# Performance work log

Hardware: AMD Instinct MI355X
Metric: run time of the kernel (lower is better)

## Reference

```python
import jax, jax.numpy as jnp
import numpy as np

N_NODES = 100000


def gcn_conv(x, edge_index, edge_weight, W, b):
    """GCNConv with self-loops and symmetric normalization: D^-1/2 (A+I) D^-1/2 (xW) + b."""
    n = x.shape[0]
    h = x @ W  # [N, out]
    src, dst = edge_index[0], edge_index[1]
    loop = jnp.arange(n, dtype=edge_index.dtype)
    src_f = jnp.concatenate([src, loop])
    dst_f = jnp.concatenate([dst, loop])
    w_f = jnp.concatenate([edge_weight, jnp.ones((n,), dtype=edge_weight.dtype)])
    deg = jax.ops.segment_sum(w_f, dst_f, num_segments=n)  # in-degree incl. self-loop
    dinv = jnp.where(deg > 0, jax.lax.rsqrt(deg), 0.0)
    norm = dinv[src_f] * w_f * dinv[dst_f]  # [E+N]
    msg = norm[:, None] * h[src_f]  # gather + scale
    out = jax.ops.segment_sum(msg, dst_f, num_segments=n)  # scatter-add
    return out + b


def setup_inputs() -> dict:
    key = jax.random.key(0)
    k1, k2, k3, k4 = jax.random.split(key, 4)
    x = jax.random.normal(k1, (N_NODES, 512), dtype=jnp.float32)
    edge_index = jax.random.randint(k2, (2, 3200000), 0, N_NODES, dtype=jnp.int64)
    edge_weight = jnp.ones((3200000,), dtype=jnp.float32)
    W1 = jax.random.normal(k3, (512, 16), dtype=jnp.float32) * 0.05
    b1 = jnp.zeros((16,), dtype=jnp.float32)
    W2 = jax.random.normal(k4, (16, 7), dtype=jnp.float32) * 0.05
    b2 = jnp.zeros((7,), dtype=jnp.float32)
    return {"x": x, "edge_index": edge_index, "edge_weight": edge_weight,
            "W1": W1, "b1": b1, "W2": W2, "b2": b2}


def reference(x, edge_index, edge_weight, W1, b1, W2, b2):
    h = jax.nn.relu(gcn_conv(x, edge_index, edge_weight, W1, b1))
    # F.dropout(training=False) is identity at inference
    h = gcn_conv(h, edge_index, edge_weight, W2, b2)
    return jax.nn.log_softmax(h, axis=1)
```

## Files before the change

kernel.cpp:

```cpp
#include <hip/hip_runtime.h>
#include <hip/hip_fp16.h>
#include <math.h>


#define F0 512
#define F1 16
#define F2 7
#define NPB 128
#define NBMAX 1024
#define BINCAP 4800
#define CH 4096
#define CMAX 80


__global__ __launch_bounds__(1024) void k_init2(
        const int* __restrict__ ei32, int twoE, int* __restrict__ flag,
        int* __restrict__ gcnt) {
    int t = threadIdx.x;
    if (t < 64) {
        int idx = 1 + 2 * t;
        int v = (idx < twoE) ? ei32[idx] : 0;
        unsigned long long b = __ballot(v != 0);
        if (t == 0) *flag = (b == 0ULL) ? 1 : 0;
    }
    if (t < NBMAX) gcnt[t] = 0;
}

__global__ __launch_bounds__(512) void kA_bin(
        const int* __restrict__ ei32, const long long* __restrict__ ei64,
        const int* __restrict__ flag, const float* __restrict__ w,
        int* __restrict__ gcnt, int2* __restrict__ binrec, int E, int nbin) {
    __shared__ int2 sorted[CH];
    __shared__ unsigned short binof[CH];
    __shared__ int hist[NBMAX];
    __shared__ int scanb[NBMAX];
    __shared__ int basel[NBMAX];
    __shared__ int curb[NBMAX];
    int t = threadIdx.x;
    int base = blockIdx.x * CH;
    int cnt_c = E - base; if (cnt_c > CH) cnt_c = CH;
    for (int i = t; i < NBMAX; i += 512) { hist[i] = 0; curb[i] = 0; }
    __syncthreads();
    bool f64 = (*flag) != 0;
#pragma unroll
    for (int k = 0; k < CH / 512; ++k) {
        int li = t + k * 512;
        if (li < cnt_c) {
            int e = base + li;
            int dst = f64 ? (int)ei64[(size_t)E + e] : ei32[(size_t)E + e];
            atomicAdd(&hist[dst >> 7], 1);
        }
    }
    __syncthreads();
    scanb[t] = hist[t]; scanb[t + 512] = hist[t + 512];
    __syncthreads();
    for (int off = 1; off < NBMAX; off <<= 1) {
        int a0 = (t >= off) ? scanb[t - off] : 0;
        int a1 = scanb[t + 512 - off];
        __syncthreads();
        scanb[t] += a0; scanb[t + 512] += a1;
        __syncthreads();
    }
    {
        int e0 = scanb[t] - hist[t];
        int e1 = scanb[t + 512] - hist[t + 512];
        __syncthreads();
        scanb[t] = e0; scanb[t + 512] = e1;
        if (t < nbin)       basel[t]       = hist[t]       ? atomicAdd(&gcnt[t],       hist[t])       : 0;
        if (t + 512 < nbin) basel[t + 512] = hist[t + 512] ? atomicAdd(&gcnt[t + 512], hist[t + 512]) : 0;
    }
    __syncthreads();
#pragma unroll
    for (int k = 0; k < CH / 512; ++k) {
        int li = t + k * 512;
        if (li < cnt_c) {
            int e = base + li;
            int src, dst;
            if (f64) { src = (int)ei64[e]; dst = (int)ei64[(size_t)E + e]; }
            else     { src = ei32[e];      dst = ei32[(size_t)E + e]; }
            int b = dst >> 7;
            int r = atomicAdd(&curb[b], 1);
            int slot = scanb[b] + r;
            sorted[slot] = make_int2((src << 7) | (dst & 127),
                                     __float_as_int(w[e]));
            binof[slot] = (unsigned short)b;
        }
    }
    __syncthreads();
    for (int idx = t; idx < cnt_c; idx += 512) {
        int b = binof[idx];
        int pos = basel[b] + (idx - scanb[b]);
        if (pos < BINCAP)
            binrec[(size_t)b * BINCAP + pos] = sorted[idx];
    }
}

__global__ __launch_bounds__(1024) void kB_scanbins(
        const int* __restrict__ gcnt, int* __restrict__ gbase, int nbin) {
    __shared__ int s[NBMAX];
    int t = threadIdx.x;
    int v = 0;
    if (t < nbin) { v = gcnt[t]; if (v > BINCAP) v = BINCAP; }
    s[t] = v;
    __syncthreads();
    for (int off = 1; off < NBMAX; off <<= 1) {
        int a = (t >= off) ? s[t - off] : 0;
        __syncthreads();
        s[t] += a;
        __syncthreads();
    }
    if (t < nbin) gbase[t] = s[t] - v;
}

__global__ __launch_bounds__(512) void kB_build(
        const int2* __restrict__ binrec, const int* __restrict__ gcnt,
        const int* __restrict__ gbase, int2* __restrict__ ep,
        int* __restrict__ rp, int* __restrict__ cntn,
        float* __restrict__ dinv, int n) {
    __shared__ int2 rec[BINCAP];
    __shared__ int2 srt[BINCAP];
    __shared__ int hist[NPB];
    __shared__ float wsum[NPB];
    __shared__ int offl[NPB];
    __shared__ int curl[NPB];
    int bin = blockIdx.x;
    int t = threadIdx.x;
    int cb = gcnt[bin]; if (cb > BINCAP) cb = BINCAP;
    int gb = gbase[bin];
    if (t < NPB) { hist[t] = 0; wsum[t] = 0.f; curl[t] = 0; }
    __syncthreads();
    for (int i = t; i < cb; i += 512) {
        int2 r = binrec[(size_t)bin * BINCAP + i];
        rec[i] = r;
        int d = r.x & 127;
        atomicAdd(&hist[d], 1);
        atomicAdd(&wsum[d], __int_as_float(r.y));
    }
    __syncthreads();
    if (t < NPB) offl[t] = hist[t];
    __syncthreads();
    for (int off = 1; off < NPB; off <<= 1) {
        int a = 0;
        if (t < NPB && t >= off) a = offl[t - off];
        __syncthreads();
        if (t < NPB) offl[t] += a;
        __syncthreads();
    }
    if (t < NPB) {
        int excl = offl[t] - hist[t];
        int node = bin * NPB + t;
        if (node < n) {
            cntn[node] = hist[t];
            rp[node] = gb + excl;
            float d = 1.f + wsum[t];
            dinv[node] = (d > 0.f) ? rsqrtf(d) : 0.f;
        }
        offl[t] = excl;
    }
    __syncthreads();
    for (int i = t; i < cb; i += 512) {
        int2 r = rec[i];
        int d = r.x & 127;
        int slot = offl[d] + atomicAdd(&curl[d], 1);
        srt[slot] = make_int2((int)(((unsigned)r.x) >> 7), r.y);
    }
    __syncthreads();
    for (int i = t; i < cb; i += 512)
        ep[(size_t)gb + i] = srt[i];
}

__global__ __launch_bounds__(256) void k_gemm1(
        const float* __restrict__ x, const float* __restrict__ W1,
        const float* __restrict__ dinv, __half* __restrict__ h1, int n) {
    int row = blockIdx.x * 256 + threadIdx.x;
    if (row >= n) return;
    const float4* xr = (const float4*)(x + (size_t)row * F0);
    const float4* wb = (const float4*)W1;
    float acc[F1];
#pragma unroll
    for (int j = 0; j < F1; ++j) acc[j] = 0.f;
#pragma unroll 2
    for (int k4 = 0; k4 < F0 / 4; ++k4) {
        float4 xv = xr[k4];
        const float4* wr = wb + k4 * 16;
#pragma unroll
        for (int j4 = 0; j4 < 4; ++j4) {
            float4 w0 = wr[j4];
            float4 w1 = wr[4 + j4];
            float4 w2 = wr[8 + j4];
            float4 w3 = wr[12 + j4];
            acc[4*j4+0] = fmaf(xv.w, w3.x, fmaf(xv.z, w2.x, fmaf(xv.y, w1.x, fmaf(xv.x, w0.x, acc[4*j4+0]))));
            acc[4*j4+1] = fmaf(xv.w, w3.y, fmaf(xv.z, w2.y, fmaf(xv.y, w1.y, fmaf(xv.x, w0.y, acc[4*j4+1]))));
            acc[4*j4+2] = fmaf(xv.w, w3.z, fmaf(xv.z, w2.z, fmaf(xv.y, w1.z, fmaf(xv.x, w0.z, acc[4*j4+2]))));
            acc[4*j4+3] = fmaf(xv.w, w3.w, fmaf(xv.z, w2.w, fmaf(xv.y, w1.w, fmaf(xv.x, w0.w, acc[4*j4+3]))));
        }
    }
    float di = dinv[row];
    __half2 hp[8];
#pragma unroll
    for (int q = 0; q < 8; ++q)
        hp[q] = __floats2half2_rn(di * acc[2*q], di * acc[2*q+1]);
    int4 o0, o1;
    o0.x = *(int*)&hp[0]; o0.y = *(int*)&hp[1]; o0.z = *(int*)&hp[2]; o0.w = *(int*)&hp[3];
    o1.x = *(int*)&hp[4]; o1.y = *(int*)&hp[5]; o1.z = *(int*)&hp[6]; o1.w = *(int*)&hp[7];
    int4* o = (int4*)(h1 + (size_t)row * F1);
    o[0] = o0;
    o[1] = o1;
}

__global__ __launch_bounds__(256) void kg1(
        const int* __restrict__ rp, const int* __restrict__ cntn,
        const int2* __restrict__ ep, const __half* __restrict__ h1,
        const float* __restrict__ dinv, const float* __restrict__ b1,
        const float* __restrict__ W2, __half* __restrict__ h2, int n) {
    __shared__ float sW[F1 * 9];
    int t = threadIdx.x;
    if (t < F1 * 8) {
        int j = t >> 3, c = t & 7;
        sW[j * 9 + c] = (c < F2) ? W2[j * F2 + c] : 0.f;
    }
    __syncthreads();
    int node = blockIdx.x * 16 + (t >> 4);
    int j = t & 15;
    if (node >= n) return;
    int start = rp[node], c = cntn[node];
    const int2* b = ep + start;
    float a0 = 0.f, a1 = 0.f, a2 = 0.f, a3 = 0.f;
    int k = 0;
    for (; k + 3 < c; k += 4) {
        int2 p0 = b[k], p1 = b[k+1], p2 = b[k+2], p3 = b[k+3];
        a0 += __int_as_float(p0.y) * __half2float(h1[(size_t)p0.x * F1 + j]);
        a1 += __int_as_float(p1.y) * __half2float(h1[(size_t)p1.x * F1 + j]);
        a2 += __int_as_float(p2.y) * __half2float(h1[(size_t)p2.x * F1 + j]);
        a3 += __int_as_float(p3.y) * __half2float(h1[(size_t)p3.x * F1 + j]);
    }
    for (; k < c; ++k) {
        int2 p = b[k];
        a0 += __int_as_float(p.y) * __half2float(h1[(size_t)p.x * F1 + j]);
    }
    float di = dinv[node];
    float self = __half2float(h1[(size_t)node * F1 + j]);
    float g = di * ((a0 + a1) + (a2 + a3) + self) + b1[j];
    g = fmaxf(g, 0.f);
    float hv[8];
#pragma unroll
    for (int cc = 0; cc < 8; ++cc) hv[cc] = g * sW[j * 9 + cc];
#pragma unroll
    for (int off = 1; off < 16; off <<= 1) {
#pragma unroll
        for (int cc = 0; cc < 8; ++cc) hv[cc] += __shfl_xor(hv[cc], off, 16);
    }
    float o = hv[0];
#pragma unroll
    for (int cc = 1; cc < 8; ++cc) if (j == cc) o = hv[cc];
    if (j < 8) h2[(size_t)node * 8 + j] = __float2half(di * o);
}

__global__ __launch_bounds__(256) void kg2(
        const int* __restrict__ rp, const int* __restrict__ cntn,
        const int2* __restrict__ ep, const __half* __restrict__ h2,
        const float* __restrict__ dinv, const float* __restrict__ b2,
        float* __restrict__ out, int n) {
    int t = threadIdx.x;
    int node = blockIdx.x * 32 + (t >> 3);
    int c = t & 7;
    if (node >= n) return;
    int start = rp[node], cd = cntn[node];
    const int2* b = ep + start;
    float a0 = 0.f, a1 = 0.f, a2 = 0.f, a3 = 0.f;
    int k = 0;
    for (; k + 3 < cd; k += 4) {
        int2 p0 = b[k], p1 = b[k+1], p2 = b[k+2], p3 = b[k+3];
        a0 += __int_as_float(p0.y) * __half2float(h2[(size_t)p0.x * 8 + c]);
        a1 += __int_as_float(p1.y) * __half2float(h2[(size_t)p1.x * 8 + c]);
        a2 += __int_as_float(p2.y) * __half2float(h2[(size_t)p2.x * 8 + c]);
        a3 += __int_as_float(p3.y) * __half2float(h2[(size_t)p3.x * 8 + c]);
    }
    for (; k < cd; ++k) {
        int2 p = b[k];
        a0 += __int_as_float(p.y) * __half2float(h2[(size_t)p.x * 8 + c]);
    }
    float di = dinv[node];
    float self = __half2float(h2[(size_t)node * 8 + c]);
    float v = di * ((a0 + a1) + (a2 + a3) + self) + ((c < F2) ? b2[c] : 0.f);
    float vm = (c < F2) ? v : -3.0e38f;
    vm = fmaxf(vm, __shfl_xor(vm, 1, 8));
    vm = fmaxf(vm, __shfl_xor(vm, 2, 8));
    vm = fmaxf(vm, __shfl_xor(vm, 4, 8));
    float ex = (c < F2) ? __expf(v - vm) : 0.f;
    float s = ex;
    s += __shfl_xor(s, 1, 8);
    s += __shfl_xor(s, 2, 8);
    s += __shfl_xor(s, 4, 8);
    float ls = __logf(s) + vm;
    if (c < F2) out[(size_t)node * F2 + c] = v - ls;
}


__global__ __launch_bounds__(256) void kf_init(
        const int* __restrict__ ei32, int twoE, int* __restrict__ flag,
        int* __restrict__ cur, int n) {
    if (blockIdx.x == 0 && threadIdx.x < 64) {
        int idx = 1 + 2 * (int)threadIdx.x;
        int v = (idx < twoE) ? ei32[idx] : 0;
        unsigned long long b = __ballot(v != 0);
        if (threadIdx.x == 0) *flag = (b == 0ULL) ? 1 : 0;
    }
    int i = blockIdx.x * 256 + threadIdx.x;
    if (i < n) cur[i] = 0;
}

__global__ __launch_bounds__(256) void kf_fill(
        const int* __restrict__ ei32, const long long* __restrict__ ei64,
        const int* __restrict__ flag, const float* __restrict__ w,
        int* __restrict__ cur, int2* __restrict__ ep, int E) {
    int e = blockIdx.x * 256 + threadIdx.x;
    if (e >= E) return;
    int src, dst;
    if (*flag) { src = (int)ei64[e]; dst = (int)ei64[(size_t)E + e]; }
    else       { src = ei32[e];      dst = ei32[(size_t)E + e]; }
    int pos = atomicAdd(&cur[dst], 1);
    if (pos < CMAX) {
        int2 p;
        p.x = src;
        p.y = __float_as_int(w[e]);
        ep[(size_t)dst * CMAX + pos] = p;
    }
}

__global__ __launch_bounds__(256) void kf_degdinv(
        const int* __restrict__ cur, const int2* __restrict__ ep,
        float* __restrict__ dinv, int n) {
    int t = threadIdx.x;
    int node = blockIdx.x * 16 + (t >> 4);
    int j = t & 15;
    if (node >= n) return;
    int c = cur[node]; if (c > CMAX) c = CMAX;
    const int2* b = ep + (size_t)node * CMAX;
    float s = 0.f;
    for (int k = j; k < c; k += 16) s += __int_as_float(b[k].y);
    s += __shfl_xor(s, 1, 16);
    s += __shfl_xor(s, 2, 16);
    s += __shfl_xor(s, 4, 16);
    s += __shfl_xor(s, 8, 16);
    if (j == 0) {
        float d = 1.f + s;
        dinv[node] = (d > 0.f) ? rsqrtf(d) : 0.f;
    }
}

__global__ __launch_bounds__(256) void kf_gather1(
        const int* __restrict__ cur, const int2* __restrict__ ep,
        const __half* __restrict__ h1, const float* __restrict__ dinv,
        const float* __restrict__ b1, const float* __restrict__ W2,
        __half* __restrict__ h2, int n) {
    __shared__ float sW[F1 * 9];
    int t = threadIdx.x;
    if (t < F1 * 8) {
        int j = t >> 3, c = t & 7;
        sW[j * 9 + c] = (c < F2) ? W2[j * F2 + c] : 0.f;
    }
    __syncthreads();
    int node = blockIdx.x * 16 + (t >> 4);
    int j = t & 15;
    if (node >= n) return;
    int c = cur[node]; if (c > CMAX) c = CMAX;
    const int2* b = ep + (size_t)node * CMAX;
    float a0 = 0.f, a1 = 0.f;
    int k = 0;
    for (; k + 1 < c; k += 2) {
        int2 p0 = b[k], p1 = b[k + 1];
        a0 += __int_as_float(p0.y) * __half2float(h1[(size_t)p0.x * F1 + j]);
        a1 += __int_as_float(p1.y) * __half2float(h1[(size_t)p1.x * F1 + j]);
    }
    if (k < c) {
        int2 p = b[k];
        a0 += __int_as_float(p.y) * __half2float(h1[(size_t)p.x * F1 + j]);
    }
    float di = dinv[node];
    float g = di * (a0 + a1 + __half2float(h1[(size_t)node * F1 + j])) + b1[j];
    g = fmaxf(g, 0.f);
    float hv[8];
#pragma unroll
    for (int cc = 0; cc < 8; ++cc) hv[cc] = g * sW[j * 9 + cc];
#pragma unroll
    for (int off = 1; off < 16; off <<= 1) {
#pragma unroll
        for (int cc = 0; cc < 8; ++cc) hv[cc] += __shfl_xor(hv[cc], off, 16);
    }
    float o = hv[0];
#pragma unroll
    for (int cc = 1; cc < 8; ++cc) if (j == cc) o = hv[cc];
    if (j < 8) h2[(size_t)node * 8 + j] = __float2half(di * o);
}

__global__ __launch_bounds__(256) void kf_gather2(
        const int* __restrict__ cur, const int2* __restrict__ ep,
        const __half* __restrict__ h2, const float* __restrict__ dinv,
        const float* __restrict__ b2, float* __restrict__ out, int n) {
    int t = threadIdx.x;
    int node = blockIdx.x * 32 + (t >> 3);
    int c = t & 7;
    if (node >= n) return;
    int cd = cur[node]; if (cd > CMAX) cd = CMAX;
    const int2* b = ep + (size_t)node * CMAX;
    float a0 = 0.f, a1 = 0.f;
    int k = 0;
    for (; k + 1 < cd; k += 2) {
        int2 p0 = b[k], p1 = b[k + 1];
        a0 += __int_as_float(p0.y) * __half2float(h2[(size_t)p0.x * 8 + c]);
        a1 += __int_as_float(p1.y) * __half2float(h2[(size_t)p1.x * 8 + c]);
    }
    if (k < cd) {
        int2 p = b[k];
        a0 += __int_as_float(p.y) * __half2float(h2[(size_t)p.x * 8 + c]);
    }
    float di = dinv[node];
    float v = di * (a0 + a1 + __half2float(h2[(size_t)node * 8 + c]))
              + ((c < F2) ? b2[c] : 0.f);
    float vm = (c < F2) ? v : -3.0e38f;
    vm = fmaxf(vm, __shfl_xor(vm, 1, 8));
    vm = fmaxf(vm, __shfl_xor(vm, 2, 8));
    vm = fmaxf(vm, __shfl_xor(vm, 4, 8));
    float ex = (c < F2) ? __expf(v - vm) : 0.f;
    float s = ex;
    s += __shfl_xor(s, 1, 8);
    s += __shfl_xor(s, 2, 8);
    s += __shfl_xor(s, 4, 8);
    float ls = __logf(s) + vm;
    if (c < F2) out[(size_t)node * F2 + c] = v - ls;
}


extern "C" void kernel_launch(void* const* d_in, const int* in_sizes, int n_in,
                              void* d_out, int out_size, void* d_ws, size_t ws_size,
                              hipStream_t stream) {
    const float* x  = (const float*)d_in[0];
    const int* ei32 = (const int*)d_in[1];
    const long long* ei64 = (const long long*)d_in[1];
    const float* w  = (const float*)d_in[2];
    const float* W1 = (const float*)d_in[3];
    const float* b1 = (const float*)d_in[4];
    const float* W2 = (const float*)d_in[5];
    const float* b2 = (const float*)d_in[6];
    float* out = (float*)d_out;

    const int n = in_sizes[0] / F0;
    const int E = in_sizes[2];
    const int B = 256;

    const int nbin = (n + NPB - 1) / NPB;
    double mean = (double)E / (double)nbin;
    bool ok_bin = (n <= (1 << 17)) && (nbin <= NBMAX) &&
                  (mean + 8.0 * sqrt(mean) + 64.0 <= (double)BINCAP);

    size_t binrec_b = (size_t)nbin * BINCAP * sizeof(int2);
    size_t alias_b  = (size_t)n * (F1 + 8) * sizeof(__half);
    size_t reg0     = binrec_b > alias_b ? binrec_b : alias_b;
    size_t need_bin = reg0 + (size_t)E * sizeof(int2)
                    + (size_t)n * 3 * 4 + (size_t)NBMAX * 8 + 256;

    if (ok_bin && ws_size >= need_bin) {
        char* p = (char*)d_ws;
        int2* binrec = (int2*)p;
        __half* h1   = (__half*)p;
        __half* h2   = h1 + (size_t)n * F1;
        int2* ep     = (int2*)(p + reg0);
        float* dinv  = (float*)(ep + E);
        int* rp      = (int*)(dinv + n);
        int* cntn    = rp + n;
        int* gcnt    = cntn + n;
        int* gbase   = gcnt + NBMAX;
        int* flag    = gbase + NBMAX;

        k_init2<<<1, 1024, 0, stream>>>(ei32, 2 * E, flag, gcnt);
        kA_bin<<<(E + CH - 1) / CH, 512, 0, stream>>>(
            ei32, ei64, flag, w, gcnt, binrec, E, nbin);
        kB_scanbins<<<1, 1024, 0, stream>>>(gcnt, gbase, nbin);
        kB_build<<<nbin, 512, 0, stream>>>(binrec, gcnt, gbase, ep, rp, cntn, dinv, n);
        k_gemm1<<<(n + 255) / 256, B, 0, stream>>>(x, W1, dinv, h1, n);
        kg1<<<(n + 15) / 16, B, 0, stream>>>(rp, cntn, ep, h1, dinv, b1, W2, h2, n);
        kg2<<<(n + 31) / 32, B, 0, stream>>>(rp, cntn, ep, h2, dinv, b2, out, n);
    } else {
        const int nbN = (n + B - 1) / B;
        const int nbE = (E + B - 1) / B;
        int2* ep    = (int2*)d_ws;
        __half* h1  = (__half*)(ep + (size_t)n * CMAX);
        __half* h2  = h1 + (size_t)n * F1;
        float* dinv = (float*)(h2 + (size_t)n * 8);
        int* cur    = (int*)(dinv + n);
        int* flag   = cur + n;

        kf_init<<<nbN, B, 0, stream>>>(ei32, 2 * E, flag, cur, n);
        kf_fill<<<nbE, B, 0, stream>>>(ei32, ei64, flag, w, cur, ep, E);
        kf_degdinv<<<(n + 15) / 16, B, 0, stream>>>(cur, ep, dinv, n);
        k_gemm1<<<(n + 255) / 256, B, 0, stream>>>(x, W1, dinv, h1, n);
        kf_gather1<<<(n + 15) / 16, B, 0, stream>>>(cur, ep, h1, dinv, b1, W2, h2, n);
        kf_gather2<<<(n + 31) / 32, B, 0, stream>>>(cur, ep, h2, dinv, b2, out, n);
    }
}
```

Before: 491.0 us.

## Aggregate directly from destination bins with shared-memory atomics, drop CSR build

Removes the per-bin counting sort that built a CSR edge list (scan kernel plus build kernel). The gather kernels now process each 128-node bin in one block, reading the unsorted bin records and accumulating into shared-memory float atomics. A separate light kernel computes degrees. The x loads in the first GEMM become nontemporal. This cuts two kernels and an edge-array write/read, at the cost of heavy LDS atomic contention and only 782 blocks of parallelism in the gather stages.

```diff
diff --git a/kernel.cpp b/kernel.cpp
--- a/kernel.cpp
+++ b/kernel.cpp
@@ -11,6 +11,8 @@
 #define BINCAP 4800
 #define CH 4096
 #define CMAX 80
+
+typedef float nt_f4 __attribute__((ext_vector_type(4)));
 
 
 __global__ __launch_bounds__(1024) void k_init2(
@@ -95,78 +97,28 @@
     }
 }
 
-__global__ __launch_bounds__(1024) void kB_scanbins(
-        const int* __restrict__ gcnt, int* __restrict__ gbase, int nbin) {
-    __shared__ int s[NBMAX];
-    int t = threadIdx.x;
-    int v = 0;
-    if (t < nbin) { v = gcnt[t]; if (v > BINCAP) v = BINCAP; }
-    s[t] = v;
-    __syncthreads();
-    for (int off = 1; off < NBMAX; off <<= 1) {
-        int a = (t >= off) ? s[t - off] : 0;
-        __syncthreads();
-        s[t] += a;
-        __syncthreads();
-    }
-    if (t < nbin) gbase[t] = s[t] - v;
-}
-
-__global__ __launch_bounds__(512) void kB_build(
+__global__ __launch_bounds__(512) void kB_deg(
         const int2* __restrict__ binrec, const int* __restrict__ gcnt,
-        const int* __restrict__ gbase, int2* __restrict__ ep,
-        int* __restrict__ rp, int* __restrict__ cntn,
         float* __restrict__ dinv, int n) {
-    __shared__ int2 rec[BINCAP];
-    __shared__ int2 srt[BINCAP];
-    __shared__ int hist[NPB];
     __shared__ float wsum[NPB];
-    __shared__ int offl[NPB];
-    __shared__ int curl[NPB];
     int bin = blockIdx.x;
     int t = threadIdx.x;
+    if (t < NPB) wsum[t] = 0.f;
+    __syncthreads();
     int cb = gcnt[bin]; if (cb > BINCAP) cb = BINCAP;
-    int gb = gbase[bin];
-    if (t < NPB) { hist[t] = 0; wsum[t] = 0.f; curl[t] = 0; }
-    __syncthreads();
+    const int2* rec = binrec + (size_t)bin * BINCAP;
     for (int i = t; i < cb; i += 512) {
-        int2 r = binrec[(size_t)bin * BINCAP + i];
-        rec[i] = r;
-        int d = r.x & 127;
-        atomicAdd(&hist[d], 1);
-        atomicAdd(&wsum[d], __int_as_float(r.y));
-    }
-    __syncthreads();
-    if (t < NPB) offl[t] = hist[t];
-    __syncthreads();
-    for (int off = 1; off < NPB; off <<= 1) {
-        int a = 0;
-        if (t < NPB && t >= off) a = offl[t - off];
-        __syncthreads();
-        if (t < NPB) offl[t] += a;
-        __syncthreads();
-    }
+        int2 r = rec[i];
+        atomicAdd(&wsum[r.x & 127], __int_as_float(r.y));
+    }
+    __syncthreads();
     if (t < NPB) {
-        int excl = offl[t] - hist[t];
         int node = bin * NPB + t;
         if (node < n) {
-            cntn[node] = hist[t];
-            rp[node] = gb + excl;
             float d = 1.f + wsum[t];
             dinv[node] = (d > 0.f) ? rsqrtf(d) : 0.f;
         }
-        offl[t] = excl;
-    }
-    __syncthreads();
-    for (int i = t; i < cb; i += 512) {
-        int2 r = rec[i];
-        int d = r.x & 127;
-        int slot = offl[d] + atomicAdd(&curl[d], 1);
-        srt[slot] = make_int2((int)(((unsigned)r.x) >> 7), r.y);
-    }
-    __syncthreads();
-    for (int i = t; i < cb; i += 512)
-        ep[(size_t)gb + i] = srt[i];
+    }
 }
 
 __global__ __launch_bounds__(256) void k_gemm1(
@@ -174,14 +126,14 @@
         const float* __restrict__ dinv, __half* __restrict__ h1, int n) {
     int row = blockIdx.x * 256 + threadIdx.x;
     if (row >= n) return;
-    const float4* xr = (const float4*)(x + (size_t)row * F0);
+    const nt_f4* xr = (const nt_f4*)(x + (size_t)row * F0);
     const float4* wb = (const float4*)W1;
     float acc[F1];
 #pragma unroll
     for (int j = 0; j < F1; ++j) acc[j] = 0.f;
 #pragma unroll 2
     for (int k4 = 0; k4 < F0 / 4; ++k4) {
-        float4 xv = xr[k4];
+        nt_f4 xv = __builtin_nontemporal_load(&xr[k4]);
         const float4* wr = wb + k4 * 16;
 #pragma unroll
         for (int j4 = 0; j4 < 4; ++j4) {
@@ -208,92 +160,121 @@
     o[1] = o1;
 }
 
-__global__ __launch_bounds__(256) void kg1(
-        const int* __restrict__ rp, const int* __restrict__ cntn,
-        const int2* __restrict__ ep, const __half* __restrict__ h1,
-        const float* __restrict__ dinv, const float* __restrict__ b1,
-        const float* __restrict__ W2, __half* __restrict__ h2, int n) {
+__global__ __launch_bounds__(512) void kbg1(
+        const int2* __restrict__ binrec, const int* __restrict__ gcnt,
+        const __half* __restrict__ h1, const float* __restrict__ dinv,
+        const float* __restrict__ b1, const float* __restrict__ W2,
+        __half* __restrict__ h2, int n) {
+    __shared__ float acc[NPB * F1];
     __shared__ float sW[F1 * 9];
     int t = threadIdx.x;
+    int bin = blockIdx.x;
+    for (int i = t; i < NPB * F1; i += 512) acc[i] = 0.f;
     if (t < F1 * 8) {
         int j = t >> 3, c = t & 7;
         sW[j * 9 + c] = (c < F2) ? W2[j * F2 + c] : 0.f;
     }
     __syncthreads();
-    int node = blockIdx.x * 16 + (t >> 4);
-    int j = t & 15;
-    if (node >= n) return;
-    int start = rp[node], c = cntn[node];
-    const int2* b = ep + start;
-    float a0 = 0.f, a1 = 0.f, a2 = 0.f, a3 = 0.f;
-    int k = 0;
-    for (; k + 3 < c; k += 4) {
-        int2 p0 = b[k], p1 = b[k+1], p2 = b[k+2], p3 = b[k+3];
-        a0 += __int_as_float(p0.y) * __half2float(h1[(size_t)p0.x * F1 + j]);
-        a1 += __int_as_float(p1.y) * __half2float(h1[(size_t)p1.x * F1 + j]);
-        a2 += __int_as_float(p2.y) * __half2float(h1[(size_t)p2.x * F1 + j]);
-        a3 += __int_as_float(p3.y) * __half2float(h1[(size_t)p3.x * F1 + j]);
-    }
-    for (; k < c; ++k) {
-        int2 p = b[k];
-        a0 += __int_as_float(p.y) * __half2float(h1[(size_t)p.x * F1 + j]);
-    }
-    float di = dinv[node];
-    float self = __half2float(h1[(size_t)node * F1 + j]);
-    float g = di * ((a0 + a1) + (a2 + a3) + self) + b1[j];
-    g = fmaxf(g, 0.f);
-    float hv[8];
-#pragma unroll
-    for (int cc = 0; cc < 8; ++cc) hv[cc] = g * sW[j * 9 + cc];
-#pragma unroll
-    for (int off = 1; off < 16; off <<= 1) {
-#pragma unroll
-        for (int cc = 0; cc < 8; ++cc) hv[cc] += __shfl_xor(hv[cc], off, 16);
-    }
-    float o = hv[0];
-#pragma unroll
-    for (int cc = 1; cc < 8; ++cc) if (j == cc) o = hv[cc];
-    if (j < 8) h2[(size_t)node * 8 + j] = __float2half(di * o);
-}
-
-__global__ __launch_bounds__(256) void kg2(
-        const int* __restrict__ rp, const int* __restrict__ cntn,
-        const int2* __restrict__ ep, const __half* __restrict__ h2,
-        const float* __restrict__ dinv, const float* __restrict__ b2,
-        float* __restrict__ out, int n) {
-    int t = threadIdx.x;
-    int node = blockIdx.x * 32 + (t >> 3);
-    int c = t & 7;
-    if (node >= n) return;
-    int start = rp[node], cd = cntn[node];
-    const int2* b = ep + start;
-    float a0 = 0.f, a1 = 0.f, a2 = 0.f, a3 = 0.f;
-    int k = 0;
-    for (; k + 3 < cd; k += 4) {
-        int2 p0 = b[k], p1 = b[k+1], p2 = b[k+2], p3 = b[k+3];
-        a0 += __int_as_float(p0.y) * __half2float(h2[(size_t)p0.x * 8 + c]);
-        a1 += __int_as_float(p1.y) * __half2float(h2[(size_t)p1.x * 8 + c]);
-        a2 += __int_as_float(p2.y) * __half2float(h2[(size_t)p2.x * 8 + c]);
-        a3 += __int_as_float(p3.y) * __half2float(h2[(size_t)p3.x * 8 + c]);
-    }
-    for (; k < cd; ++k) {
-        int2 p = b[k];
-        a0 += __int_as_float(p.y) * __half2float(h2[(size_t)p.x * 8 + c]);
-    }
-    float di = dinv[node];
-    float self = __half2float(h2[(size_t)node * 8 + c]);
-    float v = di * ((a0 + a1) + (a2 + a3) + self) + ((c < F2) ? b2[c] : 0.f);
-    float vm = (c < F2) ? v : -3.0e38f;
-    vm = fmaxf(vm, __shfl_xor(vm, 1, 8));
-    vm = fmaxf(vm, __shfl_xor(vm, 2, 8));
-    vm = fmaxf(vm, __shfl_xor(vm, 4, 8));
-    float ex = (c < F2) ? __expf(v - vm) : 0.f;
-    float s = ex;
-    s += __shfl_xor(s, 1, 8);
-    s += __shfl_xor(s, 2, 8);
-    s += __shfl_xor(s, 4, 8);
-    float ls = __logf(s) + vm;
-    if (c < F2) out[(size_t)node * F2 + c] = v - ls;
+    int cb = gcnt[bin]; if (cb > BINCAP) cb = BINCAP;
+    const int2* rec = binrec + (size_t)bin * BINCAP;
+    int g = t >> 4, j = t & 15;
+    int k = g;
+    for (; k + 32 < cb; k += 64) {
+        int2 r0 = rec[k], r1 = rec[k + 32];
+        float v0 = __int_as_float(r0.y) *
+                   __half2float(h1[(size_t)(((unsigned)r0.x) >> 7) * F1 + j]);
+        float v1 = __int_as_float(r1.y) *
+                   __half2float(h1[(size_t)(((unsigned)r1.x) >> 7) * F1 + j]);
+        atomicAdd(&acc[(r0.x & 127) * F1 + j], v0);
+        atomicAdd(&acc[(r1.x & 127) * F1 + j], v1);
+    }
+    if (k < cb) {
+        int2 r = rec[k];
+        float v = __int_as_float(r.y) *
+                  __half2float(h1[(size_t)(((unsigned)r.x) >> 7) * F1 + j]);
+        atomicAdd(&acc[(r.x & 127) * F1 + j], v);
+    }
+    __syncthreads();
+#pragma unroll
+    for (int nb = 0; nb < 4; ++nb) {
+        int dl = (t >> 4) + nb * 32;
+        int node = bin * NPB + dl;
+        bool ok = node < n;
+        float di = 0.f, self = 0.f, a = 0.f;
+        if (ok) {
+            di = dinv[node];
+            self = __half2float(h1[(size_t)node * F1 + j]);
+            a = acc[dl * F1 + j];
+        }
+        float gv = fmaxf(di * (a + self) + b1[j], 0.f);
+        float hv[8];
+#pragma unroll
+        for (int cc = 0; cc < 8; ++cc) hv[cc] = gv * sW[j * 9 + cc];
+#pragma unroll
+        for (int off = 1; off < 16; off <<= 1) {
+#pragma unroll
+            for (int cc = 0; cc < 8; ++cc) hv[cc] += __shfl_xor(hv[cc], off, 16);
+        }
+        float o = hv[0];
+#pragma unroll
+        for (int cc = 1; cc < 8; ++cc) if (j == cc) o = hv[cc];
+        if (ok && j < 8) h2[(size_t)node * 8 + j] = __float2half(di * o);
+    }
+}
+
+__global__ __launch_bounds__(512) void kbg2(
+        const int2* __restrict__ binrec, const int* __restrict__ gcnt,
+        const __half* __restrict__ h2, const float* __restrict__ dinv,
+        const float* __restrict__ b2, float* __restrict__ out, int n) {
+    __shared__ float acc[NPB * 8];
+    int t = threadIdx.x;
+    int bin = blockIdx.x;
+    for (int i = t; i < NPB * 8; i += 512) acc[i] = 0.f;
+    __syncthreads();
+    int cb = gcnt[bin]; if (cb > BINCAP) cb = BINCAP;
+    const int2* rec = binrec + (size_t)bin * BINCAP;
+    int g = t >> 3, c = t & 7;
+    int k = g;
+    for (; k + 64 < cb; k += 128) {
+        int2 r0 = rec[k], r1 = rec[k + 64];
+        float v0 = __int_as_float(r0.y) *
+                   __half2float(h2[(size_t)(((unsigned)r0.x) >> 7) * 8 + c]);
+        float v1 = __int_as_float(r1.y) *
+                   __half2float(h2[(size_t)(((unsigned)r1.x) >> 7) * 8 + c]);
+        atomicAdd(&acc[(r0.x & 127) * 8 + c], v0);
+        atomicAdd(&acc[(r1.x & 127) * 8 + c], v1);
+    }
+    if (k < cb) {
+        int2 r = rec[k];
+        float v = __int_as_float(r.y) *
+                  __half2float(h2[(size_t)(((unsigned)r.x) >> 7) * 8 + c]);
+        atomicAdd(&acc[(r.x & 127) * 8 + c], v);
+    }
+    __syncthreads();
+#pragma unroll
+    for (int nb = 0; nb < 2; ++nb) {
+        int dl = (t >> 3) + nb * 64;
+        int node = bin * NPB + dl;
+        bool ok = node < n;
+        float di = 0.f, self = 0.f, a = 0.f;
+        if (ok) {
+            di = dinv[node];
+            self = __half2float(h2[(size_t)node * 8 + c]);
+            a = acc[dl * 8 + c];
+        }
+        float v = di * (a + self) + ((c < F2) ? b2[c] : 0.f);
+        float vm = (c < F2) ? v : -3.0e38f;
+        vm = fmaxf(vm, __shfl_xor(vm, 1, 8));
+        vm = fmaxf(vm, __shfl_xor(vm, 2, 8));
+        vm = fmaxf(vm, __shfl_xor(vm, 4, 8));
+        float ex = (c < F2) ? __expf(v - vm) : 0.f;
+        float s = ex;
+        s += __shfl_xor(s, 1, 8);
+        s += __shfl_xor(s, 2, 8);
+        s += __shfl_xor(s, 4, 8);
+        float ls = __logf(s) + vm;
+        if (ok && c < F2) out[(size_t)node * F2 + c] = v - ls;
+    }
 }
 
 
@@ -455,32 +436,25 @@
                   (mean + 8.0 * sqrt(mean) + 64.0 <= (double)BINCAP);
 
     size_t binrec_b = (size_t)nbin * BINCAP * sizeof(int2);
-    size_t alias_b  = (size_t)n * (F1 + 8) * sizeof(__half);
-    size_t reg0     = binrec_b > alias_b ? binrec_b : alias_b;
-    size_t need_bin = reg0 + (size_t)E * sizeof(int2)
-                    + (size_t)n * 3 * 4 + (size_t)NBMAX * 8 + 256;
+    size_t need_bin = binrec_b + (size_t)n * (F1 + 8) * sizeof(__half)
+                    + (size_t)n * 4 + (size_t)NBMAX * 4 + 256;
 
     if (ok_bin && ws_size >= need_bin) {
         char* p = (char*)d_ws;
         int2* binrec = (int2*)p;
-        __half* h1   = (__half*)p;
+        __half* h1   = (__half*)(binrec + (size_t)nbin * BINCAP);
         __half* h2   = h1 + (size_t)n * F1;
-        int2* ep     = (int2*)(p + reg0);
-        float* dinv  = (float*)(ep + E);
-        int* rp      = (int*)(dinv + n);
-        int* cntn    = rp + n;
-        int* gcnt    = cntn + n;
-        int* gbase   = gcnt + NBMAX;
-        int* flag    = gbase + NBMAX;
+        float* dinv  = (float*)(h2 + (size_t)n * 8);
+        int* gcnt    = (int*)(dinv + n);
+        int* flag    = gcnt + NBMAX;
 
         k_init2<<<1, 1024, 0, stream>>>(ei32, 2 * E, flag, gcnt);
         kA_bin<<<(E + CH - 1) / CH, 512, 0, stream>>>(
             ei32, ei64, flag, w, gcnt, binrec, E, nbin);
-        kB_scanbins<<<1, 1024, 0, stream>>>(gcnt, gbase, nbin);
-        kB_build<<<nbin, 512, 0, stream>>>(binrec, gcnt, gbase, ep, rp, cntn, dinv, n);
+        kB_deg<<<nbin, 512, 0, stream>>>(binrec, gcnt, dinv, n);
         k_gemm1<<<(n + 255) / 256, B, 0, stream>>>(x, W1, dinv, h1, n);
-        kg1<<<(n + 15) / 16, B, 0, stream>>>(rp, cntn, ep, h1, dinv, b1, W2, h2, n);
-        kg2<<<(n + 31) / 32, B, 0, stream>>>(rp, cntn, ep, h2, dinv, b2, out, n);
+        kbg1<<<nbin, 512, 0, stream>>>(binrec, gcnt, h1, dinv, b1, W2, h2, n);
+        kbg2<<<nbin, 512, 0, stream>>>(binrec, gcnt, h2, dinv, b2, out, n);
     } else {
         const int nbN = (n + B - 1) / B;
         const int nbE = (E + B - 1) / B;
```

Result: slower. 1.008 ms (+105.4%).
